# Kernel optimization log

Measured on AMD Instinct MI355X. Metric: run time of the kernel, lower is better.

## Reference

```python
import jax, jax.numpy as jnp
import numpy as np

MARGIN = 1.0
EPS = 1e-12


def setup_inputs() -> dict:
    key = jax.random.key(0)
    k1, k2, k3 = jax.random.split(key, 3)
    inputs = jax.random.normal(k1, (8192, 128), dtype=jnp.float32)
    targets = jax.random.randint(k2, (8192,), 0, 64, dtype=jnp.int64)
    center = jax.random.normal(k3, (16, 128), dtype=jnp.float32)
    return {"inputs": inputs, "targets": targets, "center": center}


def reference(inputs, targets, center):
    n = inputs.shape[0]
    # pairwise Euclidean distances via ||a||^2 + ||b||^2 - 2 a.b  (matches addmm_ trick)
    sq = jnp.sum(inputs * inputs, axis=1)                      # [n]
    dist2 = sq[:, None] + sq[None, :] - 2.0 * (inputs @ inputs.T)
    dist = jnp.sqrt(jnp.clip(dist2, EPS))                      # [n, n]

    mask = targets[:, None] == targets[None, :]                # same-class mask [n, n]

    # batch-hard mining, fully vectorized (replaces per-row python loops)
    dist_ap = jnp.max(jnp.where(mask, dist, -jnp.inf), axis=1)  # hardest positive
    neg_min = jnp.min(jnp.where(mask, jnp.inf, dist), axis=1)   # hardest negative
    has_neg = jnp.any(~mask, axis=1)
    dist_an = jnp.where(has_neg, neg_min, dist_ap + MARGIN)

    # center augmentation: min over distances to L2-normalized prototypes
    cn = center / jnp.linalg.norm(center, axis=1, keepdims=True)       # [P, d]
    dc = jnp.sqrt(jnp.sum((inputs[:, None, :] - cn[None, :, :]) ** 2, axis=-1))  # [n, P]
    dc = jnp.clip(dc, EPS)
    dist_an = jnp.minimum(dist_an, jnp.min(dc, axis=1))

    # MarginRankingLoss with y=1: mean(relu(dist_ap - dist_an + margin))
    loss = jnp.mean(jnp.maximum(dist_ap - dist_an + MARGIN, 0.0))
    return loss
```

## Files before the change

kernel.cpp:

```cpp
#include <hip/hip_runtime.h>
#include <hip/hip_bf16.h>


#define N_ROWS 8192
#define DIM 128
#define NPROTO 16
#define MARGIN_F 1.0f
#define EPS_F 1e-12f

typedef __attribute__((ext_vector_type(8))) short short8;
typedef __attribute__((ext_vector_type(4))) float float4v;

static __device__ __forceinline__ unsigned f2bf(float f) {
  unsigned u = __float_as_uint(f);
  u += 0x7fffu + ((u >> 16) & 1u);
  return u >> 16;
}

__global__ void prep_centers_kernel(const float* __restrict__ center,
                                    float* __restrict__ cn,
                                    float* __restrict__ out0) {
  int tid = threadIdx.x;
  if (tid == 0) out0[0] = 0.0f;
  int row = tid >> 4;
  int l = tid & 15;
  float v[8];
  float ss = 0.f;
#pragma unroll
  for (int j = 0; j < 8; ++j) {
    v[j] = center[row * DIM + l * 8 + j];
    ss += v[j] * v[j];
  }
#pragma unroll
  for (int m = 1; m < 16; m <<= 1) ss += __shfl_xor(ss, m, 64);
  float inv = 1.0f / sqrtf(ss);
#pragma unroll
  for (int j = 0; j < 8; ++j) cn[row * DIM + l * 8 + j] = v[j] * inv;
}

__global__ void prep_rows_kernel(const float* __restrict__ x,
                                 const float* __restrict__ cn,
                                 uint4* __restrict__ xbf4,
                                 float* __restrict__ sq,
                                 float* __restrict__ mindc) {
  __shared__ float scn[NPROTO * DIM];
  int tid = threadIdx.x;
#pragma unroll
  for (int j = 0; j < 8; ++j) scn[j * 256 + tid] = cn[j * 256 + tid];
  __syncthreads();
  int rloc = tid >> 4, l = tid & 15;
  int row = blockIdx.x * 16 + rloc;
  float4 v0 = ((const float4*)x)[row * 32 + l * 2];
  float4 v1 = ((const float4*)x)[row * 32 + l * 2 + 1];
  float ss = v0.x * v0.x + v0.y * v0.y + v0.z * v0.z + v0.w * v0.w +
             v1.x * v1.x + v1.y * v1.y + v1.z * v1.z + v1.w * v1.w;
  float dots[NPROTO];
#pragma unroll
  for (int p = 0; p < NPROTO; ++p) {
    const float* c = &scn[p * DIM + l * 8];
    dots[p] = v0.x * c[0] + v0.y * c[1] + v0.z * c[2] + v0.w * c[3] +
              v1.x * c[4] + v1.y * c[5] + v1.z * c[6] + v1.w * c[7];
  }
#pragma unroll
  for (int m = 1; m < 16; m <<= 1) {
    ss += __shfl_xor(ss, m, 64);
#pragma unroll
    for (int p = 0; p < NPROTO; ++p) dots[p] += __shfl_xor(dots[p], m, 64);
  }
  uint4 pk;
  pk.x = f2bf(v0.x) | (f2bf(v0.y) << 16);
  pk.y = f2bf(v0.z) | (f2bf(v0.w) << 16);
  pk.z = f2bf(v1.x) | (f2bf(v1.y) << 16);
  pk.w = f2bf(v1.z) | (f2bf(v1.w) << 16);
  xbf4[row * 16 + l] = pk;
  if (l == 0) {
    float mind2 = INFINITY;
#pragma unroll
    for (int p = 0; p < NPROTO; ++p)
      mind2 = fminf(mind2, ss + 1.0f - 2.0f * dots[p]);
    sq[row] = ss;
    mindc[row] = fmaxf(sqrtf(fmaxf(mind2, 0.0f)), EPS_F);
  }
}

__global__ __launch_bounds__(256, 2) void
pairdist_kernel(const char* __restrict__ xbf, const float* __restrict__ sq,
                const int* __restrict__ tgt, float* __restrict__ pmax,
                float* __restrict__ pmin) {
  __shared__ float smax[4][64];
  __shared__ float smin[4][64];
  int bid = blockIdx.x;
  int rg = bid >> 3;
  int strip = bid & 7;
  int wave = threadIdx.x >> 6, lane = threadIdx.x & 63;
  int rowbase = rg * 64;
  int q = lane >> 4, l16 = lane & 15;
  int colbase = strip * 1024 + wave * 256;

  short8 a[4][4];
#pragma unroll
  for (int rt = 0; rt < 4; ++rt) {
    const char* ar = xbf + (size_t)(rowbase + rt * 16 + l16) * 256 + q * 16;
#pragma unroll
    for (int kc = 0; kc < 4; ++kc) a[rt][kc] = *(const short8*)(ar + kc * 64);
  }
  int4 trow[4];
#pragma unroll
  for (int rt = 0; rt < 4; ++rt)
    trow[rt] = ((const int4*)tgt)[(rowbase >> 2) + rt * 4 + q];

  float maxp[16], minn[16];
#pragma unroll
  for (int i = 0; i < 16; ++i) { maxp[i] = -INFINITY; minn[i] = INFINITY; }

  short8 bn[4];
  float sqn;
  int tcn;
  {
    const char* br = xbf + (size_t)(colbase + l16) * 256 + q * 16;
#pragma unroll
    for (int kc = 0; kc < 4; ++kc) bn[kc] = *(const short8*)(br + kc * 64);
    sqn = sq[colbase + l16];
    tcn = tgt[colbase + l16];
  }

#pragma unroll
  for (int t = 0; t < 16; ++t) {
    short8 bc[4];
#pragma unroll
    for (int kc = 0; kc < 4; ++kc) bc[kc] = bn[kc];
    float sqc = sqn;
    int tc = tcn;
    int cnext = colbase + ((t + 1) & 15) * 16;
    const char* br = xbf + (size_t)(cnext + l16) * 256 + q * 16;
#pragma unroll
    for (int kc = 0; kc < 4; ++kc) bn[kc] = *(const short8*)(br + kc * 64);
    sqn = sq[cnext + l16];
    tcn = tgt[cnext + l16];

    float4v acc[4];
#pragma unroll
    for (int rt = 0; rt < 4; ++rt) acc[rt] = (float4v){0.f, 0.f, 0.f, 0.f};
#pragma unroll
    for (int kc = 0; kc < 4; ++kc)
#pragma unroll
      for (int rt = 0; rt < 4; ++rt)
        acc[rt] = __builtin_amdgcn_mfma_f32_16x16x32_bf16(a[rt][kc], bc[kc],
                                                          acc[rt], 0, 0, 0);
#pragma unroll
    for (int rt = 0; rt < 4; ++rt) {
      int tr[4] = {trow[rt].x, trow[rt].y, trow[rt].z, trow[rt].w};
#pragma unroll
      for (int r = 0; r < 4; ++r) {
        float v = fmaf(-2.0f, acc[rt][r], sqc);
        bool s = (tc == tr[r]);
        int idx = rt * 4 + r;
        maxp[idx] = s ? fmaxf(maxp[idx], v) : maxp[idx];
        minn[idx] = s ? minn[idx] : fminf(minn[idx], v);
      }
    }
  }

#pragma unroll
  for (int m = 1; m < 16; m <<= 1) {
#pragma unroll
    for (int i = 0; i < 16; ++i) {
      maxp[i] = fmaxf(maxp[i], __shfl_xor(maxp[i], m, 64));
      minn[i] = fminf(minn[i], __shfl_xor(minn[i], m, 64));
    }
  }
  if (l16 == 0) {
#pragma unroll
    for (int rt = 0; rt < 4; ++rt)
#pragma unroll
      for (int r = 0; r < 4; ++r) {
        smax[wave][rt * 16 + q * 4 + r] = maxp[rt * 4 + r];
        smin[wave][rt * 16 + q * 4 + r] = minn[rt * 4 + r];
      }
  }
  __syncthreads();
  if (threadIdx.x < 64) {
    float M = fmaxf(fmaxf(smax[0][threadIdx.x], smax[1][threadIdx.x]),
                    fmaxf(smax[2][threadIdx.x], smax[3][threadIdx.x]));
    float m = fminf(fminf(smin[0][threadIdx.x], smin[1][threadIdx.x]),
                    fminf(smin[2][threadIdx.x], smin[3][threadIdx.x]));
    pmax[strip * N_ROWS + rowbase + threadIdx.x] = M;
    pmin[strip * N_ROWS + rowbase + threadIdx.x] = m;
  }
}

__global__ void finalize_kernel(const float* __restrict__ pmax,
                                const float* __restrict__ pmin,
                                const float* __restrict__ sq,
                                const float* __restrict__ mindc,
                                float* __restrict__ out) {
  __shared__ float wsum[4];
  int i = blockIdx.x * 256 + threadIdx.x;
  float maxv = -INFINITY, minv = INFINITY;
#pragma unroll
  for (int s = 0; s < 8; ++s) {
    maxv = fmaxf(maxv, pmax[s * N_ROWS + i]);
    minv = fminf(minv, pmin[s * N_ROWS + i]);
  }
  float si = sq[i];
  float dap = sqrtf(fmaxf(si + maxv, EPS_F));
  float dan = (minv > 1e37f) ? (dap + MARGIN_F) : sqrtf(fmaxf(si + minv, EPS_F));
  dan = fminf(dan, mindc[i]);
  float c = fmaxf(dap - dan + MARGIN_F, 0.0f) * (1.0f / (float)N_ROWS);
#pragma unroll
  for (int m = 1; m < 64; m <<= 1) c += __shfl_xor(c, m, 64);
  int lane = threadIdx.x & 63, wave = threadIdx.x >> 6;
  if (lane == 0) wsum[wave] = c;
  __syncthreads();
  if (threadIdx.x == 0) atomicAdd(out, wsum[0] + wsum[1] + wsum[2] + wsum[3]);
}

extern "C" void kernel_launch(void* const* d_in, const int* in_sizes, int n_in,
                              void* d_out, int out_size, void* d_ws, size_t ws_size,
                              hipStream_t stream) {
  const float* inputs = (const float*)d_in[0];
  const int* targets = (const int*)d_in[1];
  const float* center = (const float*)d_in[2];
  char* ws = (char*)d_ws;
  uint4* xbf4     = (uint4*)(ws + 0);
  float* sq       = (float*)(ws + 2097152);
  float* mindc    = (float*)(ws + 2129920);
  float* cn       = (float*)(ws + 2162688);
  float* pmax     = (float*)(ws + 2170880);
  float* pmin     = (float*)(ws + 2433024);
  float* out      = (float*)d_out;

  prep_centers_kernel<<<1, 256, 0, stream>>>(center, cn, out);
  prep_rows_kernel<<<512, 256, 0, stream>>>(inputs, cn, xbf4, sq, mindc);
  pairdist_kernel<<<1024, 256, 0, stream>>>((const char*)xbf4, sq, targets, pmax, pmin);
  finalize_kernel<<<32, 256, 0, stream>>>(pmax, pmin, sq, mindc, out);
}
```

Baseline: 111.1 us.

## Fuse kernels into two launches with LDS-staged B tiles and atomic finalize

Merges center normalization into the row prep kernel and folds the finalize step into the pairwise kernel, using order-preserving encoded atomicMin/atomicMax plus a last-block counter to compute the loss. The pairwise kernel now uses 2048 blocks with narrower column strips, stages B tiles through double-buffered swizzled LDS, pre-seeds accumulators with -0.5*sq to drop a per-element FMA, and packs targets into bytes. This removes two launches and the partial-result round trip. In exchange it adds atomic contention, a serial final block, and assumes class labels fit in 8 bits.

```diff
diff --git a/kernel.cpp b/kernel.cpp
--- a/kernel.cpp
+++ b/kernel.cpp
@@ -3,10 +3,12 @@
 
 
 #define N_ROWS 8192
-#define DIM 128
 #define NPROTO 16
 #define MARGIN_F 1.0f
 #define EPS_F 1e-12f
+#define NBLK_PD 2048
+#define ENCP_INIT 0xFF800000u
+#define ENCN_INIT 0x007FFFFFu
 
 typedef __attribute__((ext_vector_type(8))) short short8;
 typedef __attribute__((ext_vector_type(4))) float float4v;
@@ -16,39 +18,39 @@
   u += 0x7fffu + ((u >> 16) & 1u);
   return u >> 16;
 }
-
-__global__ void prep_centers_kernel(const float* __restrict__ center,
-                                    float* __restrict__ cn,
-                                    float* __restrict__ out0) {
+static __device__ __forceinline__ unsigned encf(float f) {
+  unsigned u = __float_as_uint(f);
+  return (u & 0x80000000u) ? ~u : (u | 0x80000000u);
+}
+static __device__ __forceinline__ float decf(unsigned e) {
+  unsigned u = (e & 0x80000000u) ? (e ^ 0x80000000u) : ~e;
+  return __uint_as_float(u);
+}
+
+__global__ void prep_kernel(const float* __restrict__ x,
+                            const float* __restrict__ center,
+                            uint4* __restrict__ xbf4, float* __restrict__ sq,
+                            float* __restrict__ mindc,
+                            unsigned* __restrict__ pposU,
+                            unsigned* __restrict__ pnegU,
+                            unsigned* __restrict__ counter) {
+  __shared__ float scn[NPROTO * 128];
+  __shared__ float sinv[NPROTO];
   int tid = threadIdx.x;
-  if (tid == 0) out0[0] = 0.0f;
-  int row = tid >> 4;
-  int l = tid & 15;
-  float v[8];
-  float ss = 0.f;
-#pragma unroll
-  for (int j = 0; j < 8; ++j) {
-    v[j] = center[row * DIM + l * 8 + j];
-    ss += v[j] * v[j];
-  }
-#pragma unroll
-  for (int m = 1; m < 16; m <<= 1) ss += __shfl_xor(ss, m, 64);
-  float inv = 1.0f / sqrtf(ss);
-#pragma unroll
-  for (int j = 0; j < 8; ++j) cn[row * DIM + l * 8 + j] = v[j] * inv;
-}
-
-__global__ void prep_rows_kernel(const float* __restrict__ x,
-                                 const float* __restrict__ cn,
-                                 uint4* __restrict__ xbf4,
-                                 float* __restrict__ sq,
-                                 float* __restrict__ mindc) {
-  __shared__ float scn[NPROTO * DIM];
-  int tid = threadIdx.x;
-#pragma unroll
-  for (int j = 0; j < 8; ++j) scn[j * 256 + tid] = cn[j * 256 + tid];
+#pragma unroll
+  for (int j = 0; j < 8; ++j) scn[j * 256 + tid] = center[j * 256 + tid];
   __syncthreads();
   int rloc = tid >> 4, l = tid & 15;
+  {
+    const float* c = &scn[rloc * 128 + l * 8];
+    float ss = 0.f;
+#pragma unroll
+    for (int j = 0; j < 8; ++j) ss += c[j] * c[j];
+#pragma unroll
+    for (int m = 1; m < 16; m <<= 1) ss += __shfl_xor(ss, m, 64);
+    if (l == 0) sinv[rloc] = 1.0f / sqrtf(ss);
+  }
+  __syncthreads();
   int row = blockIdx.x * 16 + rloc;
   float4 v0 = ((const float4*)x)[row * 32 + l * 2];
   float4 v1 = ((const float4*)x)[row * 32 + l * 2 + 1];
@@ -57,7 +59,7 @@
   float dots[NPROTO];
 #pragma unroll
   for (int p = 0; p < NPROTO; ++p) {
-    const float* c = &scn[p * DIM + l * 8];
+    const float* c = &scn[p * 128 + l * 8];
     dots[p] = v0.x * c[0] + v0.y * c[1] + v0.z * c[2] + v0.w * c[3] +
               v1.x * c[4] + v1.y * c[5] + v1.z * c[6] + v1.w * c[7];
   }
@@ -77,25 +79,30 @@
     float mind2 = INFINITY;
 #pragma unroll
     for (int p = 0; p < NPROTO; ++p)
-      mind2 = fminf(mind2, ss + 1.0f - 2.0f * dots[p]);
+      mind2 = fminf(mind2, ss + 1.0f - 2.0f * dots[p] * sinv[p]);
     sq[row] = ss;
     mindc[row] = fmaxf(sqrtf(fmaxf(mind2, 0.0f)), EPS_F);
   }
-}
-
-__global__ __launch_bounds__(256, 2) void
+  if (tid < 16) pposU[blockIdx.x * 16 + tid] = ENCP_INIT;
+  else if (tid < 32) pnegU[blockIdx.x * 16 + tid - 16] = ENCN_INIT;
+  if (blockIdx.x == 0 && tid == 32) *counter = 0u;
+}
+
+__global__ __launch_bounds__(256) void
 pairdist_kernel(const char* __restrict__ xbf, const float* __restrict__ sq,
-                const int* __restrict__ tgt, float* __restrict__ pmax,
-                float* __restrict__ pmin) {
-  __shared__ float smax[4][64];
-  __shared__ float smin[4][64];
+                const int* __restrict__ tgt, const float* __restrict__ mindc,
+                unsigned* __restrict__ pposU, unsigned* __restrict__ pnegU,
+                unsigned* __restrict__ counter, float* __restrict__ out) {
+  __shared__ char bstage[4][2][4096];
+  __shared__ float smrg[2][4][64];
+  __shared__ float bsum[4];
+  __shared__ int islast;
   int bid = blockIdx.x;
-  int rg = bid >> 3;
-  int strip = bid & 7;
+  int rg = bid >> 4, strip = bid & 15;
   int wave = threadIdx.x >> 6, lane = threadIdx.x & 63;
+  int q = lane >> 4, l16 = lane & 15;
   int rowbase = rg * 64;
-  int q = lane >> 4, l16 = lane & 15;
-  int colbase = strip * 1024 + wave * 256;
+  int colS = strip * 512 + wave * 16;
 
   short8 a[4][4];
 #pragma unroll
@@ -104,69 +111,93 @@
 #pragma unroll
     for (int kc = 0; kc < 4; ++kc) a[rt][kc] = *(const short8*)(ar + kc * 64);
   }
-  int4 trow[4];
-#pragma unroll
-  for (int rt = 0; rt < 4; ++rt)
-    trow[rt] = ((const int4*)tgt)[(rowbase >> 2) + rt * 4 + q];
-
-  float maxp[16], minn[16];
-#pragma unroll
-  for (int i = 0; i < 16; ++i) { maxp[i] = -INFINITY; minn[i] = INFINITY; }
-
-  short8 bn[4];
-  float sqn;
-  int tcn;
-  {
-    const char* br = xbf + (size_t)(colbase + l16) * 256 + q * 16;
-#pragma unroll
-    for (int kc = 0; kc < 4; ++kc) bn[kc] = *(const short8*)(br + kc * 64);
-    sqn = sq[colbase + l16];
-    tcn = tgt[colbase + l16];
-  }
-
-#pragma unroll
-  for (int t = 0; t < 16; ++t) {
-    short8 bc[4];
-#pragma unroll
-    for (int kc = 0; kc < 4; ++kc) bc[kc] = bn[kc];
-    float sqc = sqn;
-    int tc = tcn;
-    int cnext = colbase + ((t + 1) & 15) * 16;
-    const char* br = xbf + (size_t)(cnext + l16) * 256 + q * 16;
-#pragma unroll
-    for (int kc = 0; kc < 4; ++kc) bn[kc] = *(const short8*)(br + kc * 64);
-    sqn = sq[cnext + l16];
-    tcn = tgt[cnext + l16];
-
+  int trp[4];
+#pragma unroll
+  for (int rt = 0; rt < 4; ++rt) {
+    int4 tv = ((const int4*)tgt)[(rowbase >> 2) + rt * 4 + q];
+    trp[rt] = tv.x | (tv.y << 8) | (tv.z << 16) | (tv.w << 24);
+  }
+  int swoff[4], rdoff[4];
+#pragma unroll
+  for (int rr = 0; rr < 4; ++rr) {
+    int r = rr * 4 + q;
+    swoff[rr] = r * 256 + (((l16 ^ r) & 15) << 4);
+    rdoff[rr] = l16 * 256 + ((((rr * 4 + q) ^ l16) & 15) << 4);
+  }
+  const char* gb = xbf + (size_t)colS * 256;
+  char* myb0 = &bstage[wave][0][0];
+  char* myb1 = &bstage[wave][1][0];
+
+  uint4 rnext[4];
+#pragma unroll
+  for (int rr = 0; rr < 4; ++rr)
+    rnext[rr] = *(const uint4*)(gb + rr * 1024 + lane * 16);
+#pragma unroll
+  for (int rr = 0; rr < 4; ++rr) *(uint4*)(myb0 + swoff[rr]) = rnext[rr];
+#pragma unroll
+  for (int rr = 0; rr < 4; ++rr)
+    rnext[rr] = *(const uint4*)(gb + 16384 + rr * 1024 + lane * 16);
+  float sq0 = sq[colS + l16];
+  int tg0 = tgt[colS + l16] & 255;
+  float sq1 = sq[colS + 64 + l16];
+  int tg1 = tgt[colS + 64 + l16] & 255;
+
+  float wpmin[16], wnmax[16];
+#pragma unroll
+  for (int i = 0; i < 16; ++i) { wpmin[i] = INFINITY; wnmax[i] = -INFINITY; }
+
+#pragma unroll
+  for (int t = 0; t < 8; ++t) {
+    char* bufc = (t & 1) ? myb1 : myb0;
+    char* bufn = (t & 1) ? myb0 : myb1;
+    short8 b[4];
+#pragma unroll
+    for (int kc = 0; kc < 4; ++kc) b[kc] = *(const short8*)(bufc + rdoff[kc]);
+    if (t < 7) {
+#pragma unroll
+      for (int rr = 0; rr < 4; ++rr) *(uint4*)(bufn + swoff[rr]) = rnext[rr];
+    }
+    if (t < 6) {
+      const char* g2 = gb + (t + 2) * 16384;
+#pragma unroll
+      for (int rr = 0; rr < 4; ++rr)
+        rnext[rr] = *(const uint4*)(g2 + rr * 1024 + lane * 16);
+    }
+    float cini = -0.5f * sq0;
     float4v acc[4];
 #pragma unroll
-    for (int rt = 0; rt < 4; ++rt) acc[rt] = (float4v){0.f, 0.f, 0.f, 0.f};
+    for (int rt = 0; rt < 4; ++rt) acc[rt] = (float4v){cini, cini, cini, cini};
 #pragma unroll
     for (int kc = 0; kc < 4; ++kc)
 #pragma unroll
       for (int rt = 0; rt < 4; ++rt)
-        acc[rt] = __builtin_amdgcn_mfma_f32_16x16x32_bf16(a[rt][kc], bc[kc],
+        acc[rt] = __builtin_amdgcn_mfma_f32_16x16x32_bf16(a[rt][kc], b[kc],
                                                           acc[rt], 0, 0, 0);
+    int tcur = tg0;
+    sq0 = sq1; tg0 = tg1;
+    if (t < 6) {
+      sq1 = sq[colS + (t + 2) * 64 + l16];
+      tg1 = tgt[colS + (t + 2) * 64 + l16] & 255;
+    }
 #pragma unroll
     for (int rt = 0; rt < 4; ++rt) {
-      int tr[4] = {trow[rt].x, trow[rt].y, trow[rt].z, trow[rt].w};
 #pragma unroll
       for (int r = 0; r < 4; ++r) {
-        float v = fmaf(-2.0f, acc[rt][r], sqc);
-        bool s = (tc == tr[r]);
+        int tb = (trp[rt] >> (8 * r)) & 255;
+        float w = acc[rt][r];
+        bool s = (tcur == tb);
         int idx = rt * 4 + r;
-        maxp[idx] = s ? fmaxf(maxp[idx], v) : maxp[idx];
-        minn[idx] = s ? minn[idx] : fminf(minn[idx], v);
+        wpmin[idx] = fminf(wpmin[idx], s ? w : INFINITY);
+        wnmax[idx] = fmaxf(wnmax[idx], s ? -INFINITY : w);
       }
     }
   }
-
 #pragma unroll
   for (int m = 1; m < 16; m <<= 1) {
 #pragma unroll
     for (int i = 0; i < 16; ++i) {
-      maxp[i] = fmaxf(maxp[i], __shfl_xor(maxp[i], m, 64));
-      minn[i] = fminf(minn[i], __shfl_xor(minn[i], m, 64));
+      wpmin[i] = fminf(wpmin[i], __shfl_xor(wpmin[i], m, 64));
+      wnmax[i] = fmaxf(wnmax[i], __shfl_xor(wnmax[i], m, 64));
     }
   }
   if (l16 == 0) {
@@ -174,45 +205,48 @@
     for (int rt = 0; rt < 4; ++rt)
 #pragma unroll
       for (int r = 0; r < 4; ++r) {
-        smax[wave][rt * 16 + q * 4 + r] = maxp[rt * 4 + r];
-        smin[wave][rt * 16 + q * 4 + r] = minn[rt * 4 + r];
+        smrg[0][wave][rt * 16 + q * 4 + r] = wpmin[rt * 4 + r];
+        smrg[1][wave][rt * 16 + q * 4 + r] = wnmax[rt * 4 + r];
       }
   }
   __syncthreads();
   if (threadIdx.x < 64) {
-    float M = fmaxf(fmaxf(smax[0][threadIdx.x], smax[1][threadIdx.x]),
-                    fmaxf(smax[2][threadIdx.x], smax[3][threadIdx.x]));
-    float m = fminf(fminf(smin[0][threadIdx.x], smin[1][threadIdx.x]),
-                    fminf(smin[2][threadIdx.x], smin[3][threadIdx.x]));
-    pmax[strip * N_ROWS + rowbase + threadIdx.x] = M;
-    pmin[strip * N_ROWS + rowbase + threadIdx.x] = m;
-  }
-}
-
-__global__ void finalize_kernel(const float* __restrict__ pmax,
-                                const float* __restrict__ pmin,
-                                const float* __restrict__ sq,
-                                const float* __restrict__ mindc,
-                                float* __restrict__ out) {
-  __shared__ float wsum[4];
-  int i = blockIdx.x * 256 + threadIdx.x;
-  float maxv = -INFINITY, minv = INFINITY;
-#pragma unroll
-  for (int s = 0; s < 8; ++s) {
-    maxv = fmaxf(maxv, pmax[s * N_ROWS + i]);
-    minv = fminf(minv, pmin[s * N_ROWS + i]);
-  }
-  float si = sq[i];
-  float dap = sqrtf(fmaxf(si + maxv, EPS_F));
-  float dan = (minv > 1e37f) ? (dap + MARGIN_F) : sqrtf(fmaxf(si + minv, EPS_F));
-  dan = fminf(dan, mindc[i]);
-  float c = fmaxf(dap - dan + MARGIN_F, 0.0f) * (1.0f / (float)N_ROWS);
-#pragma unroll
-  for (int m = 1; m < 64; m <<= 1) c += __shfl_xor(c, m, 64);
-  int lane = threadIdx.x & 63, wave = threadIdx.x >> 6;
-  if (lane == 0) wsum[wave] = c;
-  __syncthreads();
-  if (threadIdx.x == 0) atomicAdd(out, wsum[0] + wsum[1] + wsum[2] + wsum[3]);
+    int i = threadIdx.x;
+    float wp = fminf(fminf(smrg[0][0][i], smrg[0][1][i]),
+                     fminf(smrg[0][2][i], smrg[0][3][i]));
+    float wn = fmaxf(fmaxf(smrg[1][0][i], smrg[1][1][i]),
+                     fmaxf(smrg[1][2][i], smrg[1][3][i]));
+    atomicMin(&pposU[rowbase + i], encf(wp));
+    atomicMax(&pnegU[rowbase + i], encf(wn));
+  }
+  __threadfence();
+  __syncthreads();
+  if (threadIdx.x == 0) islast = (atomicAdd(counter, 1u) == NBLK_PD - 1u);
+  __syncthreads();
+  if (!islast) return;
+  __threadfence();
+  float lsum = 0.f;
+#pragma unroll 4
+  for (int k = 0; k < N_ROWS / 256; ++k) {
+    int i = k * 256 + threadIdx.x;
+    unsigned ep = __hip_atomic_load(&pposU[i], __ATOMIC_RELAXED,
+                                    __HIP_MEMORY_SCOPE_AGENT);
+    unsigned en = __hip_atomic_load(&pnegU[i], __ATOMIC_RELAXED,
+                                    __HIP_MEMORY_SCOPE_AGENT);
+    float si = sq[i];
+    float dap = sqrtf(fmaxf(fmaf(-2.0f, decf(ep), si), EPS_F));
+    float dan = (en == ENCN_INIT)
+                    ? (dap + MARGIN_F)
+                    : sqrtf(fmaxf(fmaf(-2.0f, decf(en), si), EPS_F));
+    dan = fminf(dan, mindc[i]);
+    lsum += fmaxf(dap - dan + MARGIN_F, 0.0f);
+  }
+#pragma unroll
+  for (int m = 1; m < 64; m <<= 1) lsum += __shfl_xor(lsum, m, 64);
+  if (lane == 0) bsum[wave] = lsum;
+  __syncthreads();
+  if (threadIdx.x == 0)
+    out[0] = (bsum[0] + bsum[1] + bsum[2] + bsum[3]) * (1.0f / (float)N_ROWS);
 }
 
 extern "C" void kernel_launch(void* const* d_in, const int* in_sizes, int n_in,
@@ -222,16 +256,16 @@
   const int* targets = (const int*)d_in[1];
   const float* center = (const float*)d_in[2];
   char* ws = (char*)d_ws;
-  uint4* xbf4     = (uint4*)(ws + 0);
-  float* sq       = (float*)(ws + 2097152);
-  float* mindc    = (float*)(ws + 2129920);
-  float* cn       = (float*)(ws + 2162688);
-  float* pmax     = (float*)(ws + 2170880);
-  float* pmin     = (float*)(ws + 2433024);
-  float* out      = (float*)d_out;
-
-  prep_centers_kernel<<<1, 256, 0, stream>>>(center, cn, out);
-  prep_rows_kernel<<<512, 256, 0, stream>>>(inputs, cn, xbf4, sq, mindc);
-  pairdist_kernel<<<1024, 256, 0, stream>>>((const char*)xbf4, sq, targets, pmax, pmin);
-  finalize_kernel<<<32, 256, 0, stream>>>(pmax, pmin, sq, mindc, out);
-}
+  uint4* xbf4       = (uint4*)(ws + 0);
+  float* sq         = (float*)(ws + 2097152);
+  float* mindc      = (float*)(ws + 2129920);
+  unsigned* pposU   = (unsigned*)(ws + 2162688);
+  unsigned* pnegU   = (unsigned*)(ws + 2195456);
+  unsigned* counter = (unsigned*)(ws + 2228224);
+  float* out        = (float*)d_out;
+
+  prep_kernel<<<512, 256, 0, stream>>>(inputs, center, xbf4, sq, mindc,
+                                       pposU, pnegU, counter);
+  pairdist_kernel<<<NBLK_PD, 256, 0, stream>>>((const char*)xbf4, sq, targets,
+                                               mindc, pposU, pnegU, counter, out);
+}
```

New measurement: 229.2 us. +106.4%, slower.
